# Kernel optimization log

Hardware: AMD Instinct MI355X
Metric: run time of the kernel (lower is better)

Reference implementation:

```python
import jax, jax.numpy as jnp
import numpy as np

B, DIM, H, W = 4, 192, 128, 128
HEADS = 4
K_RATES = (1.0 / 2, 2.0 / 3, 3.0 / 4, 4.0 / 5)


def setup_inputs() -> dict:
    key = jax.random.key(0)
    ks = jax.random.split(key, 5)
    x = jax.random.normal(ks[0], (B, DIM, H, W), jnp.float32)
    w_qkv = jax.random.normal(ks[1], (3 * DIM, DIM, 1, 1), jnp.float32) * 0.05
    w_dw = jax.random.normal(ks[2], (3 * DIM, 1, 3, 3), jnp.float32) * 0.05
    w_proj = jax.random.normal(ks[3], (DIM, DIM, 1, 1), jnp.float32) * 0.05
    temperature = jnp.ones((HEADS, 1, 1), jnp.float32)
    attn_w = jnp.full((4,), 0.2, jnp.float32)
    return {"x": x, "w_qkv": w_qkv, "w_dw": w_dw, "w_proj": w_proj,
            "temperature": temperature, "attn_w": attn_w}


def _conv1x1(x, w):
    # x: [b,c,h,w], w: [o,c,1,1]
    return jnp.einsum('bchw,oc->bohw', x, w[:, :, 0, 0])


def _dwconv3x3(x, w):
    # depthwise 3x3, padding=1; w: [c,1,3,3]
    return jax.lax.conv_general_dilated(
        x, w, window_strides=(1, 1), padding=((1, 1), (1, 1)),
        dimension_numbers=('NCHW', 'OIHW', 'NCHW'),
        feature_group_count=x.shape[1])


def _l2norm(x, eps=1e-12):
    # matches F.normalize(dim=-1): x / max(||x||, eps)
    n = jnp.sqrt(jnp.sum(x * x, axis=-1, keepdims=True))
    return x / jnp.maximum(n, eps)


def reference(x, w_qkv, w_dw, w_proj, temperature, attn_w):
    b, c, h, w = x.shape
    qkv = _dwconv3x3(_conv1x1(x, w_qkv), w_dw)  # [b, 3c, h, w]
    q, k, v = jnp.split(qkv, 3, axis=1)

    def heads(t):
        return t.reshape(b, HEADS, c // HEADS, h * w)  # [b, head, C, hw]

    q, k, v = heads(q), heads(k), heads(v)
    q = _l2norm(q)
    k = _l2norm(k)

    C = q.shape[2]
    attn = jnp.einsum('bhcn,bhdn->bhcd', q, k) * temperature[None]  # [b,head,C,C]

    out = jnp.zeros_like(v)
    for i, rate in enumerate(K_RATES):
        k_val = max(1, int(C * rate))
        _, idx = jax.lax.top_k(attn, k_val)  # [b,head,C,k]
        mask = jax.nn.one_hot(idx, C, dtype=attn.dtype).sum(axis=-2)  # [b,head,C,C]
        branch = jnp.where(mask > 0, attn, -jnp.inf)
        branch = jax.nn.softmax(branch, axis=-1)
        out = out + jnp.einsum('bhcd,bhdn->bhcn', branch, v) * attn_w[i]

    out = out.reshape(b, c, h, w)
    return _conv1x1(out, w_proj)
```

## Files before the change

### kernel.cpp

```cpp
#include <hip/hip_runtime.h>
#include <math.h>
#include <stdint.h>

#define BB 4
#define DIM 192
#define HEADS 4
#define CH 48
#define HW 16384
#define C3 576
#define NCHUNK 64

typedef unsigned short ushort_t;
typedef __attribute__((ext_vector_type(8))) short short8;
typedef __attribute__((ext_vector_type(4))) float floatx4;

__device__ __forceinline__ float bf2f(unsigned int u) {
    union { unsigned int i; float f; } v; v.i = u << 16; return v.f;
}
__device__ __forceinline__ ushort_t f2bf(float f) {
    union { float f; unsigned int i; } v; v.f = f;
    unsigned int x = v.i;
    x += 0x7fffu + ((x >> 16) & 1u);
    return (ushort_t)(x >> 16);
}

__global__ __launch_bounds__(256) void zero_init(float* __restrict__ p, int n) {
    int i = blockIdx.x * 256 + threadIdx.x;
    if (i < n) p[i] = 0.f;
}

__global__ __launch_bounds__(256) void convert_split(
    const float* __restrict__ in, ushort_t* __restrict__ hi,
    ushort_t* __restrict__ lo, int n)
{
    int i = blockIdx.x * 256 + threadIdx.x;
    if (i < n) {
        float f = in[i];
        ushort_t h = f2bf(f);
        hi[i] = h;
        lo[i] = f2bf(f - bf2f(h));
    }
}

__global__ __launch_bounds__(256) void tconv(
    const float* __restrict__ in, ushort_t* __restrict__ out_hi,
    ushort_t* __restrict__ out_lo, long inStride)
{
    int z = blockIdx.z;
    in += (long)z * inStride;
    out_hi += (long)z * HW * DIM;
    out_lo += (long)z * HW * DIM;
    __shared__ ushort_t th[64][80];
    __shared__ ushort_t tl[64][80];
    int n0 = blockIdx.x * 64, k0 = blockIdx.y * 64;
    int t = threadIdx.x;
#pragma unroll
    for (int i = 0; i < 4; ++i) {
        int kl = (t >> 4) + 16 * i;
        float4 v = *(const float4*)(in + (long)(k0 + kl) * HW + n0 + (t & 15) * 4);
        int nl = (t & 15) * 4;
        ushort_t hx = f2bf(v.x), hy = f2bf(v.y), hz = f2bf(v.z), hw = f2bf(v.w);
        th[nl + 0][kl] = hx; th[nl + 1][kl] = hy;
        th[nl + 2][kl] = hz; th[nl + 3][kl] = hw;
        tl[nl + 0][kl] = f2bf(v.x - bf2f(hx));
        tl[nl + 1][kl] = f2bf(v.y - bf2f(hy));
        tl[nl + 2][kl] = f2bf(v.z - bf2f(hz));
        tl[nl + 3][kl] = f2bf(v.w - bf2f(hw));
    }
    __syncthreads();
#pragma unroll
    for (int i = 0; i < 2; ++i) {
        int nl = t >> 2, seg = (t & 3) + 4 * i;
        *(uint4*)(out_hi + (long)(n0 + nl) * DIM + k0 + seg * 8) = *(uint4*)&th[nl][seg * 8];
        *(uint4*)(out_lo + (long)(n0 + nl) * DIM + k0 + seg * 8) = *(uint4*)&tl[nl][seg * 8];
    }
}

__global__ __launch_bounds__(256) void tconv_b16(
    const ushort_t* __restrict__ in, ushort_t* __restrict__ out)
{
    int z = blockIdx.z;
    in  += (long)z * DIM * HW;
    out += (long)z * HW * DIM;
    __shared__ ushort_t th[64][80];
    int n0 = blockIdx.x * 64, k0 = blockIdx.y * 64;
    int t = threadIdx.x;
#pragma unroll
    for (int i = 0; i < 4; ++i) {
        int kl = (t >> 4) + 16 * i;
        uint2 v = *(const uint2*)(in + (long)(k0 + kl) * HW + n0 + (t & 15) * 4);
        int nl = (t & 15) * 4;
        th[nl + 0][kl] = (ushort_t)(v.x & 0xffffu);
        th[nl + 1][kl] = (ushort_t)(v.x >> 16);
        th[nl + 2][kl] = (ushort_t)(v.y & 0xffffu);
        th[nl + 3][kl] = (ushort_t)(v.y >> 16);
    }
    __syncthreads();
#pragma unroll
    for (int i = 0; i < 2; ++i) {
        int nl = t >> 2, seg = (t & 3) + 4 * i;
        *(uint4*)(out + (long)(n0 + nl) * DIM + k0 + seg * 8) = *(uint4*)&th[nl][seg * 8];
    }
}

#define BS_STRIDE 104
template<int TERMS>
__global__ __launch_bounds__(256) void gemm_reg(
    const ushort_t* __restrict__ Ahi, const ushort_t* __restrict__ Alo,
    const ushort_t* __restrict__ BThi, const ushort_t* __restrict__ BTlo,
    float* __restrict__ C, int M, int N,
    long strideA, long strideB, long strideC)
{
    int z = blockIdx.z;
    Ahi += z * strideA; Alo += z * strideA;
    BThi += z * strideB; BTlo += z * strideB;
    C += z * strideC;
    __shared__ ushort_t Bs0[128 * BS_STRIDE];
    __shared__ ushort_t Bs1[128 * BS_STRIDE];
    int t = threadIdx.x;
    int wave = t >> 6, lane = t & 63;
    int l15 = lane & 15, quad = lane >> 4;
    int m0 = blockIdx.y * 64, n0 = blockIdx.x * 128;
    int wm = (wave & 1) * 32, wn = (wave >> 1) * 64;
    floatx4 acc[2][4];
#pragma unroll
    for (int i = 0; i < 2; ++i)
#pragma unroll
        for (int j = 0; j < 4; ++j) acc[i][j] = (floatx4){0.f, 0.f, 0.f, 0.f};

    if (TERMS == 1) {
        short8 af[2][6];
#pragma unroll
        for (int mi = 0; mi < 2; ++mi)
#pragma unroll
            for (int k0 = 0; k0 < 6; ++k0)
                af[mi][k0] = *(const short8*)(Ahi
                    + (long)(m0 + wm + mi * 16 + l15) * 192 + k0 * 32 + quad * 8);
        for (int i = t; i < 3072; i += 256) {
            int r = i / 24, seg = i % 24;
            uint4 v = *(const uint4*)(BThi + (long)(n0 + r) * 192 + seg * 8);
            ushort_t* dst = (seg < 12) ? &Bs0[r * BS_STRIDE + seg * 8]
                                       : &Bs1[r * BS_STRIDE + (seg - 12) * 8];
            *(uint4*)dst = v;
        }
        __syncthreads();
#pragma unroll
        for (int k0 = 0; k0 < 6; ++k0) {
            int ks = k0 * 32 + quad * 8;
            const ushort_t* buf = (ks < 96) ? Bs0 : Bs1;
            int col = (ks < 96) ? ks : ks - 96;
            short8 bf[4];
#pragma unroll
            for (int ni = 0; ni < 4; ++ni)
                bf[ni] = *(const short8*)&buf[(wn + ni * 16 + l15) * BS_STRIDE + col];
#pragma unroll
            for (int mi = 0; mi < 2; ++mi)
#pragma unroll
                for (int ni = 0; ni < 4; ++ni)
                    acc[mi][ni] = __builtin_amdgcn_mfma_f32_16x16x32_bf16(
                        af[mi][k0], bf[ni], acc[mi][ni], 0, 0, 0);
        }
    } else {
#pragma unroll
        for (int kh = 0; kh < 2; ++kh) {
            short8 ah[2][3], al[2][3];
#pragma unroll
            for (int mi = 0; mi < 2; ++mi)
#pragma unroll
                for (int k0 = 0; k0 < 3; ++k0) {
                    long off = (long)(m0 + wm + mi * 16 + l15) * 192
                             + kh * 96 + k0 * 32 + quad * 8;
                    ah[mi][k0] = *(const short8*)(Ahi + off);
                    al[mi][k0] = *(const short8*)(Alo + off);
                }
            if (kh) __syncthreads();
            for (int i = t; i < 1536; i += 256) {
                int r = i / 12, seg = i % 12;
                long goff = (long)(n0 + r) * 192 + kh * 96 + seg * 8;
                *(uint4*)&Bs0[r * BS_STRIDE + seg * 8] = *(const uint4*)(BThi + goff);
                *(uint4*)&Bs1[r * BS_STRIDE + seg * 8] = *(const uint4*)(BTlo + goff);
            }
            __syncthreads();
#pragma unroll
            for (int k0 = 0; k0 < 3; ++k0) {
                int col = k0 * 32 + quad * 8;
                short8 bh[4], bl[4];
#pragma unroll
                for (int ni = 0; ni < 4; ++ni) {
                    bh[ni] = *(const short8*)&Bs0[(wn + ni * 16 + l15) * BS_STRIDE + col];
                    bl[ni] = *(const short8*)&Bs1[(wn + ni * 16 + l15) * BS_STRIDE + col];
                }
#pragma unroll
                for (int mi = 0; mi < 2; ++mi)
#pragma unroll
                    for (int ni = 0; ni < 4; ++ni) {
                        acc[mi][ni] = __builtin_amdgcn_mfma_f32_16x16x32_bf16(
                            ah[mi][k0], bh[ni], acc[mi][ni], 0, 0, 0);
                        acc[mi][ni] = __builtin_amdgcn_mfma_f32_16x16x32_bf16(
                            ah[mi][k0], bl[ni], acc[mi][ni], 0, 0, 0);
                        acc[mi][ni] = __builtin_amdgcn_mfma_f32_16x16x32_bf16(
                            al[mi][k0], bh[ni], acc[mi][ni], 0, 0, 0);
                    }
            }
        }
    }
#pragma unroll
    for (int mi = 0; mi < 2; ++mi)
#pragma unroll
        for (int ni = 0; ni < 4; ++ni) {
            long base = (long)(m0 + wm + mi * 16 + quad * 4) * N + n0 + wn + ni * 16 + l15;
#pragma unroll
            for (int r = 0; r < 4; ++r)
                C[base + (long)r * N] = acc[mi][ni][r];
        }
}

__global__ __launch_bounds__(256) void dwconv3x3_lds(
    const float* __restrict__ in, const float* __restrict__ w,
    ushort_t* __restrict__ qk_hi, ushort_t* __restrict__ qk_lo,
    ushort_t* __restrict__ vbuf16, float* __restrict__ normsq,
    int c0, int chunk)
{
    __shared__ float tile[10][132];
    int z = blockIdx.z;
    int cl = blockIdx.y;
    int gc = c0 + cl;
    in  += (long)z * chunk * HW + (long)cl * HW;
    int y0 = blockIdx.x * 8;
    const float* wc = w + gc * 9;
    float wf[9];
#pragma unroll
    for (int i = 0; i < 9; ++i) wf[i] = wc[i];
    int t = threadIdx.x;
    if (t < 10) { tile[t][0] = 0.f; tile[t][129] = 0.f; }
    for (int i = t; i < 320; i += 256) {
        int r = i >> 5, c4 = (i & 31) * 4;
        int gy = y0 - 1 + r;
        float4 v = {0.f, 0.f, 0.f, 0.f};
        if (gy >= 0 && gy < 128) v = *(const float4*)(in + gy * 128 + c4);
        tile[r][1 + c4] = v.x; tile[r][2 + c4] = v.y;
        tile[r][3 + c4] = v.z; tile[r][4 + c4] = v.w;
    }
    __syncthreads();
    int yl = t >> 5, xl = (t & 31) * 4;
    float s0 = 0.f, s1 = 0.f, s2 = 0.f, s3 = 0.f;
#pragma unroll
    for (int r = 0; r < 3; ++r) {
        float c0v = tile[yl + r][xl + 0], c1v = tile[yl + r][xl + 1];
        float c2v = tile[yl + r][xl + 2], c3v = tile[yl + r][xl + 3];
        float c4v = tile[yl + r][xl + 4], c5v = tile[yl + r][xl + 5];
        float w0 = wf[r * 3], w1 = wf[r * 3 + 1], w2 = wf[r * 3 + 2];
        s0 += w0 * c0v + w1 * c1v + w2 * c2v;
        s1 += w0 * c1v + w1 * c2v + w2 * c3v;
        s2 += w0 * c2v + w1 * c3v + w2 * c4v;
        s3 += w0 * c3v + w1 * c4v + w2 * c5v;
    }
    long pix = (long)(y0 + yl) * 128 + xl;
    ushort_t h0 = f2bf(s0), h1 = f2bf(s1), h2 = f2bf(s2), h3 = f2bf(s3);
    uint2 ph;
    ph.x = (unsigned)h0 | ((unsigned)h1 << 16);
    ph.y = (unsigned)h2 | ((unsigned)h3 << 16);
    if (gc < 2 * DIM) {
        ushort_t l0 = f2bf(s0 - bf2f(h0)), l1 = f2bf(s1 - bf2f(h1));
        ushort_t l2 = f2bf(s2 - bf2f(h2)), l3 = f2bf(s3 - bf2f(h3));
        uint2 pl;
        pl.x = (unsigned)l0 | ((unsigned)l1 << 16);
        pl.y = (unsigned)l2 | ((unsigned)l3 << 16);
        long rbase = ((long)z * 384 + gc) * HW + pix;
        *(uint2*)(qk_hi + rbase) = ph;
        *(uint2*)(qk_lo + rbase) = pl;
        __syncthreads();
        float* red = (float*)tile;
        red[t] = s0 * s0 + s1 * s1 + s2 * s2 + s3 * s3;
        __syncthreads();
        for (int off = 128; off > 0; off >>= 1) {
            if (t < off) red[t] += red[t + off];
            __syncthreads();
        }
        if (t == 0) atomicAdd(&normsq[z * 512 + gc], red[0]);
    } else {
        *(uint2*)(vbuf16 + ((long)z * DIM + (gc - 2 * DIM)) * HW + pix) = ph;
    }
}

__global__ __launch_bounds__(256) void attn_mfma(
    const ushort_t* __restrict__ qk_hi, const ushort_t* __restrict__ qk_lo,
    float* __restrict__ partial)
{
    int z = blockIdx.z, h = blockIdx.y, pidx = blockIdx.x;
    int t = threadIdx.x;
    int wave = t >> 6, lane = t & 63;
    int l15 = lane & 15, quad = lane >> 4;
    long base = (long)z * 384 * HW;
    const ushort_t* qh = qk_hi + base + (long)(h * CH) * HW;
    const ushort_t* ql = qk_lo + base + (long)(h * CH) * HW;
    const ushort_t* kh = qk_hi + base + (long)(DIM + h * CH) * HW;
    const ushort_t* kl = qk_lo + base + (long)(DIM + h * CH) * HW;
    int ncol0 = pidx * 256 + wave * 64;

    floatx4 acc[3][3];
#pragma unroll
    for (int i = 0; i < 3; ++i)
#pragma unroll
        for (int j = 0; j < 3; ++j) acc[i][j] = (floatx4){0.f, 0.f, 0.f, 0.f};

#pragma unroll
    for (int ks = 0; ks < 2; ++ks) {
        int col = ncol0 + ks * 32 + quad * 8;
        short8 ah[3], al[3], bh[3], bl[3];
#pragma unroll
        for (int i = 0; i < 3; ++i) {
            long ro = (long)(i * 16 + l15) * HW + col;
            ah[i] = *(const short8*)(qh + ro);
            al[i] = *(const short8*)(ql + ro);
            bh[i] = *(const short8*)(kh + ro);
            bl[i] = *(const short8*)(kl + ro);
        }
#pragma unroll
        for (int mi = 0; mi < 3; ++mi)
#pragma unroll
            for (int ni = 0; ni < 3; ++ni) {
                acc[mi][ni] = __builtin_amdgcn_mfma_f32_16x16x32_bf16(
                    ah[mi], bh[ni], acc[mi][ni], 0, 0, 0);
                acc[mi][ni] = __builtin_amdgcn_mfma_f32_16x16x32_bf16(
                    ah[mi], bl[ni], acc[mi][ni], 0, 0, 0);
                acc[mi][ni] = __builtin_amdgcn_mfma_f32_16x16x32_bf16(
                    al[mi], bh[ni], acc[mi][ni], 0, 0, 0);
            }
    }

    __shared__ float sred[2][48 * 50];
    float* sb = sred[wave & 1];
    if (wave < 2) {
#pragma unroll
        for (int mi = 0; mi < 3; ++mi)
#pragma unroll
            for (int ni = 0; ni < 3; ++ni)
#pragma unroll
                for (int r = 0; r < 4; ++r)
                    sb[(mi * 16 + quad * 4 + r) * 50 + ni * 16 + l15] = acc[mi][ni][r];
    }
    __syncthreads();
    if (wave >= 2) {
#pragma unroll
        for (int mi = 0; mi < 3; ++mi)
#pragma unroll
            for (int ni = 0; ni < 3; ++ni)
#pragma unroll
                for (int r = 0; r < 4; ++r)
                    sb[(mi * 16 + quad * 4 + r) * 50 + ni * 16 + l15] += acc[mi][ni][r];
    }
    __syncthreads();
    float* pp = partial + ((long)(pidx * 16 + z * HEADS + h)) * 2304;
    for (int i = t; i < 2304; i += 256) {
        int row = i / 48, colo = i - row * 48;
        pp[i] = sred[0][row * 50 + colo] + sred[1][row * 50 + colo];
    }
}

__global__ __launch_bounds__(256) void topk_combine2(
    const float* __restrict__ partial, const float* __restrict__ normsq,
    const float* __restrict__ temp, const float* __restrict__ attn_w,
    float* __restrict__ Wc)
{
    int z = blockIdx.y;
    int wave = threadIdx.x >> 6, lane = threadIdx.x & 63;
    int rid = blockIdx.x * 4 + wave;
    int c = rid % CH, h = rid / CH;
    int d = lane;
    float a = -INFINITY;
    if (d < 48) {
        float s = 0.f;
        const float* pp = partial + (long)(z * HEADS + h) * 2304 + c * CH + d;
        for (int p = 0; p < NCHUNK; ++p) s += pp[(long)p * 16 * 2304];
        float invq = 1.0f / fmaxf(sqrtf(normsq[z * 512 + h * CH + c]), 1e-12f);
        float invk = 1.0f / fmaxf(sqrtf(normsq[z * 512 + DIM + h * CH + d]), 1e-12f);
        a = s * invq * invk * temp[h];
    }
    float m = a;
#pragma unroll
    for (int off = 32; off > 0; off >>= 1) m = fmaxf(m, __shfl_xor(m, off, 64));
    float e = (d < 48) ? expf(a - m) : 0.f;
    int rank = 0;
    for (int j = 0; j < 48; ++j) {
        float aj = __shfl(a, j, 64);
        rank += (aj > a) || (aj == a && j < d);
    }
    const int kv[4] = {24, 32, 36, 38};
    float s = 0.f;
#pragma unroll
    for (int i = 0; i < 4; ++i) {
        float contrib = (d < 48 && rank < kv[i]) ? e : 0.f;
#pragma unroll
        for (int off = 32; off > 0; off >>= 1) contrib += __shfl_xor(contrib, off, 64);
        s += (rank < kv[i]) ? attn_w[i] / contrib : 0.f;
    }
    if (d < 48) Wc[(long)z * 9216 + (long)rid * CH + d] = e * s;
}

__global__ __launch_bounds__(256) void build_m(
    const float* __restrict__ wproj, const float* __restrict__ Wc,
    ushort_t* __restrict__ Mb)
{
    int z = blockIdx.y;
    int idx = blockIdx.x * 256 + threadIdx.x;
    if (idx >= DIM * DIM) return;
    int cg = idx % DIM;
    int o  = idx / DIM;
    int h = cg / CH, d = cg % CH;
    const float* wp = wproj + o * DIM + h * CH;
    const float* wcc = Wc + (long)z * 9216 + (long)h * CH * CH + d;
    float s = 0.f;
#pragma unroll
    for (int ch = 0; ch < CH; ++ch) s += wp[ch] * wcc[ch * CH];
    Mb[(long)z * DIM * DIM + idx] = f2bf(s);
}

extern "C" void kernel_launch(void* const* d_in, const int* in_sizes, int n_in,
                              void* d_out, int out_size, void* d_ws, size_t ws_size,
                              hipStream_t stream) {
    const float* x      = (const float*)d_in[0];
    const float* w_qkv  = (const float*)d_in[1];
    const float* w_dw   = (const float*)d_in[2];
    const float* w_proj = (const float*)d_in[3];
    const float* temper = (const float*)d_in[4];
    const float* attn_w = (const float*)d_in[5];
    float* out = (float*)d_out;

    char* p = (char*)d_ws;
    ushort_t* qk_hi  = (ushort_t*)p;   p += (long)BB * 384 * HW * 2;
    ushort_t* qk_lo  = (ushort_t*)p;   p += (long)BB * 384 * HW * 2;
    ushort_t* vbuf16 = (ushort_t*)p;   p += (long)BB * DIM * HW * 2;
    ushort_t* xT_hi  = (ushort_t*)p;   p += (long)BB * HW * DIM * 2;
    ushort_t* xT_lo  = (ushort_t*)p;   p += (long)BB * HW * DIM * 2;
    ushort_t* wq_hi  = (ushort_t*)p;   p += (long)C3 * DIM * 2;
    ushort_t* wq_lo  = (ushort_t*)p;   p += (long)C3 * DIM * 2;
    float* normsq    = (float*)p;      p += (long)BB * 512 * 4;
    float* Wc        = (float*)p;      p += (long)BB * 9216 * 4;
    ushort_t* Mb     = (ushort_t*)p;   p += (long)BB * DIM * DIM * 2;
    float* pre       = (float*)p;
    float* partial   = pre;
    long avail = (long)ws_size - (long)(p - (char*)d_ws);
    int chunk = 64;
    if (avail >= (long)BB * 192 * HW * 4) chunk = 192;

    zero_init<<<(BB * 512 + 255) / 256, 256, 0, stream>>>(normsq, BB * 512);
    convert_split<<<(C3 * DIM + 255) / 256, 256, 0, stream>>>(
        w_qkv, wq_hi, wq_lo, C3 * DIM);
    tconv<<<dim3(HW / 64, DIM / 64, BB), 256, 0, stream>>>(
        x, xT_hi, xT_lo, (long)DIM * HW);

    for (int c0 = 0; c0 < C3; c0 += chunk) {
        if (c0 < 2 * DIM)
            gemm_reg<3><<<dim3(HW / 128, chunk / 64, BB), 256, 0, stream>>>(
                wq_hi + (long)c0 * DIM, wq_lo + (long)c0 * DIM, xT_hi, xT_lo,
                pre, chunk, HW, 0L, (long)HW * DIM, (long)chunk * HW);
        else
            gemm_reg<1><<<dim3(HW / 128, chunk / 64, BB), 256, 0, stream>>>(
                wq_hi + (long)c0 * DIM, wq_hi + (long)c0 * DIM, xT_hi, xT_hi,
                pre, chunk, HW, 0L, (long)HW * DIM, (long)chunk * HW);
        dwconv3x3_lds<<<dim3(16, chunk, BB), 256, 0, stream>>>(
            pre, w_dw, qk_hi, qk_lo, vbuf16, normsq, c0, chunk);
    }
    attn_mfma<<<dim3(NCHUNK, HEADS, BB), 256, 0, stream>>>(qk_hi, qk_lo, partial);
    topk_combine2<<<dim3(48, BB), 256, 0, stream>>>(
        partial, normsq, temper, attn_w, Wc);
    build_m<<<dim3((DIM * DIM + 255) / 256, BB), 256, 0, stream>>>(w_proj, Wc, Mb);
    tconv_b16<<<dim3(HW / 64, DIM / 64, BB), 256, 0, stream>>>(vbuf16, xT_hi);
    gemm_reg<1><<<dim3(HW / 128, DIM / 64, BB), 256, 0, stream>>>(
        Mb, Mb, xT_hi, xT_hi, out, DIM, HW,
        (long)DIM * DIM, (long)HW * DIM, (long)DIM * HW);
}
```

Baseline: 370.2 us.

## Make single-term GEMM persistent over four N-tiles with register-prefetched B loads

The TERMS==1 GEMM path now has each block handle four consecutive 128-column tiles instead of one. The A fragments stay in registers across the tiles, and the next B tile is prefetched from global memory into registers while MFMAs run on the current LDS tile. Grids for the V-projection GEMM and the final projection GEMM shrink by four. This amortizes A loads and block launch cost and overlaps global loads with compute. In exchange it uses more registers (twelve uint4 prefetch registers), adds extra barriers per tile, and leaves fewer blocks to fill the CUs.

```diff
diff --git a/kernel.cpp b/kernel.cpp
--- a/kernel.cpp
+++ b/kernel.cpp
@@ -104,6 +104,7 @@
 }
 
 #define BS_STRIDE 104
+#define BS_HALF (128 * BS_STRIDE)
 template<int TERMS>
 __global__ __launch_bounds__(256) void gemm_reg(
     const ushort_t* __restrict__ Ahi, const ushort_t* __restrict__ Alo,
@@ -115,20 +116,18 @@
     Ahi += z * strideA; Alo += z * strideA;
     BThi += z * strideB; BTlo += z * strideB;
     C += z * strideC;
-    __shared__ ushort_t Bs0[128 * BS_STRIDE];
-    __shared__ ushort_t Bs1[128 * BS_STRIDE];
+    __shared__ ushort_t Bs[2 * BS_HALF];
+    ushort_t* Bs0 = Bs;
+    ushort_t* Bs1 = Bs + BS_HALF;
     int t = threadIdx.x;
     int wave = t >> 6, lane = t & 63;
     int l15 = lane & 15, quad = lane >> 4;
-    int m0 = blockIdx.y * 64, n0 = blockIdx.x * 128;
+    int m0 = blockIdx.y * 64;
     int wm = (wave & 1) * 32, wn = (wave >> 1) * 64;
     floatx4 acc[2][4];
-#pragma unroll
-    for (int i = 0; i < 2; ++i)
-#pragma unroll
-        for (int j = 0; j < 4; ++j) acc[i][j] = (floatx4){0.f, 0.f, 0.f, 0.f};
 
     if (TERMS == 1) {
+        int n0 = blockIdx.x * 512;
         short8 af[2][6];
 #pragma unroll
         for (int mi = 0; mi < 2; ++mi)
@@ -136,31 +135,75 @@
             for (int k0 = 0; k0 < 6; ++k0)
                 af[mi][k0] = *(const short8*)(Ahi
                     + (long)(m0 + wm + mi * 16 + l15) * 192 + k0 * 32 + quad * 8);
-        for (int i = t; i < 3072; i += 256) {
+        int gof[12], dsti[12];
+#pragma unroll
+        for (int j = 0; j < 12; ++j) {
+            int i = t + j * 256;
             int r = i / 24, seg = i % 24;
-            uint4 v = *(const uint4*)(BThi + (long)(n0 + r) * 192 + seg * 8);
-            ushort_t* dst = (seg < 12) ? &Bs0[r * BS_STRIDE + seg * 8]
-                                       : &Bs1[r * BS_STRIDE + (seg - 12) * 8];
-            *(uint4*)dst = v;
+            gof[j] = r * 192 + seg * 8;
+            dsti[j] = ((seg < 12) ? 0 : BS_HALF) + r * BS_STRIDE + (seg % 12) * 8;
         }
+        uint4 sreg[12];
+#pragma unroll
+        for (int j = 0; j < 12; ++j)
+            sreg[j] = *(const uint4*)(BThi + (long)n0 * 192 + gof[j]);
+#pragma unroll
+        for (int j = 0; j < 12; ++j)
+            *(uint4*)&Bs[dsti[j]] = sreg[j];
         __syncthreads();
 #pragma unroll
-        for (int k0 = 0; k0 < 6; ++k0) {
-            int ks = k0 * 32 + quad * 8;
-            const ushort_t* buf = (ks < 96) ? Bs0 : Bs1;
-            int col = (ks < 96) ? ks : ks - 96;
-            short8 bf[4];
-#pragma unroll
-            for (int ni = 0; ni < 4; ++ni)
-                bf[ni] = *(const short8*)&buf[(wn + ni * 16 + l15) * BS_STRIDE + col];
+        for (int tt = 0; tt < 4; ++tt) {
+            int nt0 = n0 + tt * 128;
+            if (tt < 3) {
+                long nb = (long)(nt0 + 128) * 192;
+#pragma unroll
+                for (int j = 0; j < 12; ++j)
+                    sreg[j] = *(const uint4*)(BThi + nb + gof[j]);
+            }
+#pragma unroll
+            for (int i = 0; i < 2; ++i)
+#pragma unroll
+                for (int j = 0; j < 4; ++j) acc[i][j] = (floatx4){0.f, 0.f, 0.f, 0.f};
+#pragma unroll
+            for (int k0 = 0; k0 < 6; ++k0) {
+                int ks = k0 * 32 + quad * 8;
+                const ushort_t* buf = (ks < 96) ? Bs0 : Bs1;
+                int col = (ks < 96) ? ks : ks - 96;
+                short8 bf[4];
+#pragma unroll
+                for (int ni = 0; ni < 4; ++ni)
+                    bf[ni] = *(const short8*)&buf[(wn + ni * 16 + l15) * BS_STRIDE + col];
+#pragma unroll
+                for (int mi = 0; mi < 2; ++mi)
+#pragma unroll
+                    for (int ni = 0; ni < 4; ++ni)
+                        acc[mi][ni] = __builtin_amdgcn_mfma_f32_16x16x32_bf16(
+                            af[mi][k0], bf[ni], acc[mi][ni], 0, 0, 0);
+            }
 #pragma unroll
             for (int mi = 0; mi < 2; ++mi)
 #pragma unroll
-                for (int ni = 0; ni < 4; ++ni)
-                    acc[mi][ni] = __builtin_amdgcn_mfma_f32_16x16x32_bf16(
-                        af[mi][k0], bf[ni], acc[mi][ni], 0, 0, 0);
+                for (int ni = 0; ni < 4; ++ni) {
+                    long base = (long)(m0 + wm + mi * 16 + quad * 4) * N
+                              + nt0 + wn + ni * 16 + l15;
+#pragma unroll
+                    for (int r = 0; r < 4; ++r)
+                        C[base + (long)r * N] = acc[mi][ni][r];
+                }
+            if (tt < 3) {
+                __syncthreads();
+#pragma unroll
+                for (int j = 0; j < 12; ++j)
+                    *(uint4*)&Bs[dsti[j]] = sreg[j];
+                __syncthreads();
+            }
         }
     } else {
+        int n0 = blockIdx.x * 128;
+#pragma unroll
+        for (int i = 0; i < 2; ++i)
+#pragma unroll
+            for (int j = 0; j < 4; ++j) acc[i][j] = (floatx4){0.f, 0.f, 0.f, 0.f};
 #pragma unroll
         for (int kh = 0; kh < 2; ++kh) {
             short8 ah[2][3], al[2][3];
@@ -203,16 +246,17 @@
                     }
             }
         }
-    }
-#pragma unroll
-    for (int mi = 0; mi < 2; ++mi)
-#pragma unroll
-        for (int ni = 0; ni < 4; ++ni) {
-            long base = (long)(m0 + wm + mi * 16 + quad * 4) * N + n0 + wn + ni * 16 + l15;
-#pragma unroll
-            for (int r = 0; r < 4; ++r)
-                C[base + (long)r * N] = acc[mi][ni][r];
-        }
+#pragma unroll
+        for (int mi = 0; mi < 2; ++mi)
+#pragma unroll
+            for (int ni = 0; ni < 4; ++ni) {
+                long base = (long)(m0 + wm + mi * 16 + quad * 4) * N
+                          + n0 + wn + ni * 16 + l15;
+#pragma unroll
+                for (int r = 0; r < 4; ++r)
+                    C[base + (long)r * N] = acc[mi][ni][r];
+            }
+    }
 }
 
 __global__ __launch_bounds__(256) void dwconv3x3_lds(
@@ -456,7 +500,7 @@
                 wq_hi + (long)c0 * DIM, wq_lo + (long)c0 * DIM, xT_hi, xT_lo,
                 pre, chunk, HW, 0L, (long)HW * DIM, (long)chunk * HW);
         else
-            gemm_reg<1><<<dim3(HW / 128, chunk / 64, BB), 256, 0, stream>>>(
+            gemm_reg<1><<<dim3(HW / 512, chunk / 64, BB), 256, 0, stream>>>(
                 wq_hi + (long)c0 * DIM, wq_hi + (long)c0 * DIM, xT_hi, xT_hi,
                 pre, chunk, HW, 0L, (long)HW * DIM, (long)chunk * HW);
         dwconv3x3_lds<<<dim3(16, chunk, BB), 256, 0, stream>>>(
@@ -467,7 +511,7 @@
         partial, normsq, temper, attn_w, Wc);
     build_m<<<dim3((DIM * DIM + 255) / 256, BB), 256, 0, stream>>>(w_proj, Wc, Mb);
     tconv_b16<<<dim3(HW / 64, DIM / 64, BB), 256, 0, stream>>>(vbuf16, xT_hi);
-    gemm_reg<1><<<dim3(HW / 128, DIM / 64, BB), 256, 0, stream>>>(
+    gemm_reg<1><<<dim3(HW / 512, DIM / 64, BB), 256, 0, stream>>>(
         Mb, Mb, xT_hi, xT_hi, out, DIM, HW,
         (long)DIM * DIM, (long)HW * DIM, (long)DIM * HW);
 }
```

Result: slower. 416.0 us (+12.4%).
